# Kernel optimization log

Hardware: AMD Instinct MI355X
Metric: run time of the kernel (lower is better)

The kernel has to match this reference:

```python
import jax, jax.numpy as jnp
import numpy as np

B, S, H, N, L = 256, 64, 512, 16, 2
OUT_BITS = 32            # ceil(log2(n)), n = 2**32
PTR_BITS = 6             # ceil(log2(seq_len)), seq_len = 64
OUT_DIM = 3 + PTR_BITS   # = 9
T = 2 * OUT_BITS - 1     # 63 sequential decode steps


def _ln(x, g, b):
    m = jnp.mean(x, -1, keepdims=True)
    v = jnp.mean((x - m) ** 2, -1, keepdims=True)
    return (x - m) * jax.lax.rsqrt(v + 1e-5) * g + b


def _s4_step(A, Bm, Cm, D, oW, ob, s, x):
    # diagonal-SSM S4 block step: s (B,H,N) recurrent state, x (B,H) input
    s2 = A * s + Bm * x[:, :, None]
    y = jnp.einsum('bhn,hn->bh', s2, Cm) + D * x
    y = jax.nn.gelu(y, approximate=False) @ oW + ob
    return s2, y


def _forward(input_seq, in_W, in_b, A, Bm, Cm, D, outW, outb, ln_g, ln_b, head_W, head_b):
    Bsz = input_seq.shape[0]
    dt = input_seq.dtype
    x = input_seq @ in_W + in_b            # (B,S,H)
    encoded = x                            # encoded_inputs saved before S4 stack
    # ---- encoder: L S4 blocks, residual + layernorm ----
    for j in range(L):
        def step(s, xt, j=j):
            return _s4_step(A[j], Bm[j], Cm[j], D[j], outW[j], outb[j], s, xt)
        s0 = jnp.zeros((Bsz, H, N), dt)
        _, ys = jax.lax.scan(step, s0, jnp.swapaxes(x, 0, 1))
        x = _ln(jnp.swapaxes(ys, 0, 1) + x, ln_g[j], ln_b[j])
    dec0 = jnp.broadcast_to(jnp.array([0.0, 0.0, 1.0], dt), (Bsz, 3))
    carry0 = (jnp.zeros((L, Bsz, H, N), dt), jnp.zeros((Bsz, H), dt), dec0)
    ones1 = jnp.ones((Bsz, 1), dt)

    def dstep(carry, i):
        states, ctx, dec_in = carry
        dp = dec_in @ in_W + in_b          # (B,H)
        xd = dp
        new_states = []
        for j in range(L):
            s2, y = _s4_step(A[j], Bm[j], Cm[j], D[j], outW[j], outb[j], states[j], xd)
            new_states.append(s2)
            res = jnp.where(i == 0, dp, y)   # torch code: residual=proj on step 0, else doubles x_dec
            xd = _ln(y + res, ln_g[j], ln_b[j])
        is_out = (i % 2) == 0
        # pointer retrieval (only applied on odd steps via where)
        o_ptr = jax.nn.sigmoid((xd + ctx) @ head_W + head_b)
        ptr = jnp.argmax(o_ptr[:, 3:3 + PTR_BITS], axis=1)            # (B,)
        ptr_vec = jnp.take_along_axis(encoded, ptr[:, None, None], axis=1)[:, 0]
        ctx = jnp.where(is_out, ctx, ctx + ptr_vec)
        out = jax.nn.sigmoid((xd + ctx) @ head_W + head_b)            # (B,OUT_DIM)
        next_char = jnp.where(is_out, (out[:, 0:1] > 0.5).astype(dt), jnp.zeros((Bsz, 1), dt))
        tag0 = jnp.where(is_out, 1.0, 0.0) * ones1
        tag1 = ones1 - tag0
        dec_next = jnp.concatenate([next_char, tag0, tag1], axis=1)   # (B,3)
        return (jnp.stack(new_states), ctx, dec_next), out

    _, outs = jax.lax.scan(dstep, carry0, jnp.arange(T))
    return jnp.swapaxes(outs, 0, 1)        # (B, T, OUT_DIM)


def setup_inputs() -> dict:
    ks = jax.random.split(jax.random.key(0), 8)
    f32 = jnp.float32
    return {
        'input_seq': jax.random.uniform(ks[0], (B, S, 3), f32),
        'autoregressive_steps': T,
        'in_W': jax.random.normal(ks[1], (3, H), f32) * 0.5,
        'in_b': jnp.zeros((H,), f32),
        'A': jax.random.uniform(ks[2], (L, H, N), f32, 0.5, 0.99),
        'Bm': jax.random.normal(ks[3], (L, H, N), f32) * 0.1,
        'Cm': jax.random.normal(ks[4], (L, H, N), f32) * 0.1,
        'D': jnp.ones((L, H), f32),
        'outW': jax.random.normal(ks[5], (L, H, H), f32) * 0.02,
        'outb': jnp.zeros((L, H), f32),
        'ln_g': jnp.ones((L, H), f32),
        'ln_b': jnp.zeros((L, H), f32),
        'head_W': jax.random.normal(ks[6], (H, OUT_DIM), f32) * 0.05,
        'head_b': jnp.zeros((OUT_DIM,), f32),
    }


def reference(input_seq, autoregressive_steps, in_W, in_b, A, Bm, Cm, D, outW, outb, ln_g, ln_b, head_W, head_b):
    return _forward(input_seq, in_W, in_b, A, Bm, Cm, D, outW, outb, ln_g, ln_b, head_W, head_b)
```

## Files before the change

kernel.cpp:

```cpp
#include <hip/hip_runtime.h>
#include <math.h>

#define HDIM   512
#define NDIM   16
#define SEQ    64
#define TSTEPS 63
#define BATCH  256
#define ODIM   9
#define NTHR   512


__device__ __forceinline__ float gelu_f32(float x) {
    return 0.5f * x * (1.0f + erff(x * 0.70710678118654752440f));
}

__device__ __forceinline__ float sig32(float x) {
    return 1.0f / (1.0f + expf(-x));
}

__device__ __forceinline__ void load3_l2(const float* p0, const float* p1,
                                         const float* p2,
                                         float& v0, float& v1, float& v2) {
    asm volatile(
        "global_load_dword %0, %3, off sc0\n\t"
        "global_load_dword %1, %4, off sc0\n\t"
        "global_load_dword %2, %5, off sc0\n\t"
        "s_waitcnt vmcnt(0)"
        : "=&v"(v0), "=&v"(v1), "=&v"(v2)
        : "v"(p0), "v"(p1), "v"(p2)
        : "memory");
}
__device__ __forceinline__ float load1_l2(const float* p) {
    float v;
    asm volatile("global_load_dword %0, %1, off sc0\n\t"
                 "s_waitcnt vmcnt(0)"
                 : "=v"(v) : "v"(p) : "memory");
    return v;
}

__global__ __launch_bounds__(NTHR, 2)
void s4_decode_kernel(
    const float* __restrict__ input_seq,
    const float* __restrict__ in_W,
    const float* __restrict__ in_b,
    const float* __restrict__ Aarr,
    const float* __restrict__ Barr,
    const float* __restrict__ Carr,
    const float* __restrict__ Darr,
    const float* __restrict__ outW,
    const float* __restrict__ outb,
    const float* __restrict__ ln_g,
    const float* __restrict__ ln_b,
    const float* __restrict__ headW,
    const float* __restrict__ headb,
    float* __restrict__ out,
    float* gws, float* zws,
    unsigned* fg, unsigned* fz,
    unsigned* fx, unsigned* xid)
{
    __shared__ float  ld_xd[HDIM];
    __shared__ float  ld_gall[4 * HDIM];
    __shared__ float4 ld_z4[16 * 4 * 32];
    __shared__ float  ld_D0[HDIM];
    __shared__ float  ld_D1[HDIM];
    __shared__ float  ld_red[16];
    __shared__ float  ld_hred[8 * ODIM];
    __shared__ float  ld_logit[ODIM + 1];
    __shared__ float  ld_dec[4];
    __shared__ int    ld_ptr;
    __shared__ int    ld_fast;

    const int b    = blockIdx.x;
    const int tid  = threadIdx.x;
    const int hg   = tid >> 4;
    const int n    = tid & 15;
    const int mem  = (b >> 3) & 3;
    const int gbase = b - 8 * mem;
    const int c4   = tid & 31;
    const int rg   = tid >> 5;
    const int rgE  = (rg + ((b * 5) & 15)) & 15;
    const int base_row = rgE * 32;
    const int j0 = 0 + (0 >= mem), j1 = 1 + (1 >= mem), j2 = 2 + (2 >= mem);

    unsigned myxcd;
    asm volatile("s_getreg_b32 %0, hwreg(HW_REG_XCC_ID)" : "=s"(myxcd));
    if (tid == 0) {
        __hip_atomic_store(&xid[b], myxcd, __ATOMIC_RELAXED, __HIP_MEMORY_SCOPE_AGENT);
        __hip_atomic_store(&fx[b], 1u, __ATOMIC_RELEASE, __HIP_MEMORY_SCOPE_AGENT);
        unsigned ok = 1;
        #pragma unroll
        for (int j = 0; j < 4; ++j) {
            if (j == mem) continue;
            while (__hip_atomic_load(&fx[gbase + 8 * j],
                                     __ATOMIC_ACQUIRE, __HIP_MEMORY_SCOPE_AGENT) == 0)
                __builtin_amdgcn_s_sleep(1);
            ok &= (__hip_atomic_load(&xid[gbase + 8 * j],
                                     __ATOMIC_RELAXED, __HIP_MEMORY_SCOPE_AGENT) == myxcd);
        }
        ld_fast = (int)ok;
    }

    float s0[16], s1[16];
    float A0[16], B0[16], C0[16], A1[16], B1[16], C1[16];
    #pragma unroll
    for (int k = 0; k < 16; ++k) {
        int h  = hg + 32 * k;
        int i0 = h * NDIM + n;
        int i1 = (HDIM + h) * NDIM + n;
        A0[k] = Aarr[i0]; B0[k] = Barr[i0]; C0[k] = Carr[i0];
        A1[k] = Aarr[i1]; B1[k] = Barr[i1]; C1[k] = Carr[i1];
        s0[k] = 0.f; s1[k] = 0.f;
    }

    const float inb_t = in_b[tid];
    const float w0 = in_W[tid], w1 = in_W[HDIM + tid], w2 = in_W[2 * HDIM + tid];
    const float ob0 = outb[tid], ob1 = outb[HDIM + tid];
    const float lg0 = ln_g[tid], lg1 = ln_g[HDIM + tid];
    const float lb0 = ln_b[tid], lb1 = ln_b[HDIM + tid];

    ld_D0[tid] = Darr[tid];
    ld_D1[tid] = Darr[HDIM + tid];

    const float4* Wsl = (const float4*)outW + mem * 32 + c4;

    float ctxr = 0.f;
    if (tid == 0) { ld_dec[0] = 0.f; ld_dec[1] = 0.f; ld_dec[2] = 1.f; }
    __syncthreads();
    const bool fast = (ld_fast != 0);

    for (int i = 0; i < TSTEPS; ++i) {
        float dpv = fmaf(ld_dec[0], w0, fmaf(ld_dec[1], w1, fmaf(ld_dec[2], w2, inb_t)));
        __syncthreads();
        ld_xd[tid] = dpv;
        __syncthreads();

        #pragma unroll 1
        for (int blk = 0; blk < 2; ++blk) {
            const unsigned seq = (unsigned)(2 * i + blk + 1);
            {
                float* s  = blk ? s1 : s0;
                float* Ar = blk ? A1 : A0;
                float* Br = blk ? B1 : B0;
                float* Cr = blk ? C1 : C0;
                const float* Dl = blk ? ld_D1 : ld_D0;
                #pragma unroll
                for (int k = 0; k < 16; ++k) {
                    int h = hg + 32 * k;
                    float xh = ld_xd[h];
                    float sv = fmaf(Ar[k], s[k], Br[k] * xh);
                    s[k] = sv;
                    float p = sv * Cr[k];
                    p += __shfl_xor(p, 1);
                    p += __shfl_xor(p, 2);
                    p += __shfl_xor(p, 4);
                    p += __shfl_xor(p, 8);
                    if (n == 0) ld_gall[mem * HDIM + h] = gelu_f32(p + Dl[h] * xh);
                }
            }
            __syncthreads();
            if (fast) {
                gws[b * HDIM + tid] = ld_gall[mem * HDIM + tid];
            } else {
                __hip_atomic_store(&gws[b * HDIM + tid], ld_gall[mem * HDIM + tid],
                                   __ATOMIC_RELAXED, __HIP_MEMORY_SCOPE_AGENT);
            }
            __syncthreads();
            if (tid == 4)
                __hip_atomic_store(&fg[b], seq, __ATOMIC_RELAXED, __HIP_MEMORY_SCOPE_AGENT);
            if (tid < 3) {
                int j = tid + (tid >= mem ? 1 : 0);
                while (__hip_atomic_load(&fg[gbase + 8 * j],
                                         __ATOMIC_RELAXED, __HIP_MEMORY_SCOPE_AGENT) < seq)
                    __builtin_amdgcn_s_sleep(1);
            }
            __syncthreads();
            if (fast) {
                float v0, v1, v2;
                load3_l2(&gws[(gbase + 8 * j0) * HDIM + tid],
                         &gws[(gbase + 8 * j1) * HDIM + tid],
                         &gws[(gbase + 8 * j2) * HDIM + tid], v0, v1, v2);
                ld_gall[j0 * HDIM + tid] = v0;
                ld_gall[j1 * HDIM + tid] = v1;
                ld_gall[j2 * HDIM + tid] = v2;
            } else {
                ld_gall[j0 * HDIM + tid] =
                    __hip_atomic_load(&gws[(gbase + 8 * j0) * HDIM + tid],
                                      __ATOMIC_RELAXED, __HIP_MEMORY_SCOPE_AGENT);
                ld_gall[j1 * HDIM + tid] =
                    __hip_atomic_load(&gws[(gbase + 8 * j1) * HDIM + tid],
                                      __ATOMIC_RELAXED, __HIP_MEMORY_SCOPE_AGENT);
                ld_gall[j2 * HDIM + tid] =
                    __hip_atomic_load(&gws[(gbase + 8 * j2) * HDIM + tid],
                                      __ATOMIC_RELAXED, __HIP_MEMORY_SCOPE_AGENT);
            }
            __syncthreads();
            {
                const float4* Wb = Wsl + (size_t)blk * HDIM * 128;
                float4 acc[4];
                #pragma unroll
                for (int bi = 0; bi < 4; ++bi) acc[bi] = make_float4(0.f, 0.f, 0.f, 0.f);
                float4 a0 = Wb[(size_t)(base_row)     * 128];
                float4 a1 = Wb[(size_t)(base_row + 1) * 128];
                #pragma unroll 2
                for (int rr = 0; rr < 32; rr += 4) {
                    int rB = base_row + ((rr + 2) & 31);
                    float4 b0 = Wb[(size_t)rB * 128];
                    float4 b1 = Wb[(size_t)(rB + 1) * 128];
                    {
                        int r = base_row + rr;
                        #pragma unroll
                        for (int bi = 0; bi < 4; ++bi) {
                            float g0 = ld_gall[bi * HDIM + r];
                            float g1 = ld_gall[bi * HDIM + r + 1];
                            acc[bi].x = fmaf(g1, a1.x, fmaf(g0, a0.x, acc[bi].x));
                            acc[bi].y = fmaf(g1, a1.y, fmaf(g0, a0.y, acc[bi].y));
                            acc[bi].z = fmaf(g1, a1.z, fmaf(g0, a0.z, acc[bi].z));
                            acc[bi].w = fmaf(g1, a1.w, fmaf(g0, a0.w, acc[bi].w));
                        }
                    }
                    int rA = base_row + ((rr + 4) & 31);
                    a0 = Wb[(size_t)rA * 128];
                    a1 = Wb[(size_t)(rA + 1) * 128];
                    {
                        int r = base_row + rr + 2;
                        #pragma unroll
                        for (int bi = 0; bi < 4; ++bi) {
                            float g0 = ld_gall[bi * HDIM + r];
                            float g1 = ld_gall[bi * HDIM + r + 1];
                            acc[bi].x = fmaf(g1, b1.x, fmaf(g0, b0.x, acc[bi].x));
                            acc[bi].y = fmaf(g1, b1.y, fmaf(g0, b0.y, acc[bi].y));
                            acc[bi].z = fmaf(g1, b1.z, fmaf(g0, b0.z, acc[bi].z));
                            acc[bi].w = fmaf(g1, b1.w, fmaf(g0, b0.w, acc[bi].w));
                        }
                    }
                }
                #pragma unroll
                for (int bi = 0; bi < 4; ++bi)
                    ld_z4[(rg * 4 + bi) * 32 + c4] = acc[bi];
            }
            __syncthreads();
            {
                const float* zf = (const float*)ld_z4;
                int bi2 = tid >> 7;
                int col = tid & 127;
                float zv = 0.f;
                #pragma unroll
                for (int k = 0; k < 16; ++k) zv += zf[(k * 4 + bi2) * 128 + col];
                float* zp = &zws[(gbase + 8 * bi2) * HDIM + mem * 128 + col];
                if (fast) *zp = zv;
                else __hip_atomic_store(zp, zv, __ATOMIC_RELAXED, __HIP_MEMORY_SCOPE_AGENT);
            }
            __syncthreads();
            if (tid == 4)
                __hip_atomic_store(&fz[b], seq, __ATOMIC_RELAXED, __HIP_MEMORY_SCOPE_AGENT);
            if (tid < 3) {
                int j = tid + (tid >= mem ? 1 : 0);
                while (__hip_atomic_load(&fz[gbase + 8 * j],
                                         __ATOMIC_RELAXED, __HIP_MEMORY_SCOPE_AGENT) < seq)
                    __builtin_amdgcn_s_sleep(1);
            }
            __syncthreads();
            {
                float zraw = fast ? load1_l2(&zws[b * HDIM + tid])
                                  : __hip_atomic_load(&zws[b * HDIM + tid],
                                                      __ATOMIC_RELAXED,
                                                      __HIP_MEMORY_SCOPE_AGENT);
                float z = zraw + (blk ? ob1 : ob0);
                float res = (i == 0) ? dpv : z;
                float tmp = z + res;
                float v1 = tmp, v2 = tmp * tmp;
                #pragma unroll
                for (int m = 1; m < 64; m <<= 1) {
                    v1 += __shfl_xor(v1, m);
                    v2 += __shfl_xor(v2, m);
                }
                if ((tid & 63) == 0) {
                    ld_red[2 * (tid >> 6)]     = v1;
                    ld_red[2 * (tid >> 6) + 1] = v2;
                }
                __syncthreads();
                float s1r = 0.f, s2r = 0.f;
                #pragma unroll
                for (int q = 0; q < 8; ++q) { s1r += ld_red[2*q]; s2r += ld_red[2*q+1]; }
                float mu  = s1r * (1.f / 512.f);
                float var = s2r * (1.f / 512.f) - mu * mu;
                float rs  = rsqrtf(var + 1e-5f);
                __syncthreads();
                ld_xd[tid] = (tmp - mu) * rs * (blk ? lg1 : lg0) + (blk ? lb1 : lb0);
                __syncthreads();
            }
        }

        {
            float v = ld_xd[tid] + ctxr;
            const float* w = headW + tid * ODIM;
            float p[ODIM];
            #pragma unroll
            for (int o = 0; o < ODIM; ++o) p[o] = v * w[o];
            #pragma unroll
            for (int m = 1; m < 64; m <<= 1) {
                #pragma unroll
                for (int o = 0; o < ODIM; ++o) p[o] += __shfl_xor(p[o], m);
            }
            if ((tid & 63) == 0) {
                int wv = tid >> 6;
                #pragma unroll
                for (int o = 0; o < ODIM; ++o) ld_hred[wv * ODIM + o] = p[o];
            }
            __syncthreads();
            if (tid < ODIM) {
                float s = headb[tid];
                #pragma unroll
                for (int wv = 0; wv < 8; ++wv) s += ld_hred[wv * ODIM + tid];
                ld_logit[tid] = s;
            }
            __syncthreads();
        }

        const bool is_out = ((i & 1) == 0);
        if (is_out) {
            if (tid < ODIM)
                out[(b * TSTEPS + i) * ODIM + tid] = sig32(ld_logit[tid]);
            if (tid == 0) {
                float nc = (sig32(ld_logit[0]) > 0.5f) ? 1.f : 0.f;
                ld_dec[0] = nc; ld_dec[1] = 1.f; ld_dec[2] = 0.f;
            }
            __syncthreads();
        } else {
            if (tid == 0) {
                int best = 0; float bv = sig32(ld_logit[3]);
                #pragma unroll
                for (int o = 1; o < 6; ++o) {
                    float v2 = sig32(ld_logit[3 + o]);
                    if (v2 > bv) { bv = v2; best = o; }
                }
                ld_ptr = best;
                ld_dec[0] = 0.f; ld_dec[1] = 0.f; ld_dec[2] = 1.f;
            }
            __syncthreads();
            {
                const float* iseq = input_seq + (b * SEQ + ld_ptr) * 3;
                float e0 = iseq[0], e1 = iseq[1], e2 = iseq[2];
                ctxr += fmaf(e0, w0, fmaf(e1, w1, fmaf(e2, w2, inb_t)));
            }
            __syncthreads();
            {
                float v = ld_xd[tid] + ctxr;
                const float* w = headW + tid * ODIM;
                float p[ODIM];
                #pragma unroll
                for (int o = 0; o < ODIM; ++o) p[o] = v * w[o];
                #pragma unroll
                for (int m = 1; m < 64; m <<= 1) {
                    #pragma unroll
                    for (int o = 0; o < ODIM; ++o) p[o] += __shfl_xor(p[o], m);
                }
                if ((tid & 63) == 0) {
                    int wv = tid >> 6;
                    #pragma unroll
                    for (int o = 0; o < ODIM; ++o) ld_hred[wv * ODIM + o] = p[o];
                }
                __syncthreads();
                if (tid < ODIM) {
                    float s = headb[tid];
                    #pragma unroll
                    for (int wv = 0; wv < 8; ++wv) s += ld_hred[wv * ODIM + tid];
                    out[(b * TSTEPS + i) * ODIM + tid] = sig32(s);
                }
            }
            __syncthreads();
        }
    }
}

extern "C" void kernel_launch(void* const* d_in, const int* in_sizes, int n_in,
                              void* d_out, int out_size, void* d_ws, size_t ws_size,
                              hipStream_t stream) {
    (void)in_sizes; (void)n_in; (void)ws_size; (void)out_size;
    const float* input_seq = (const float*)d_in[0];
    const float* in_W   = (const float*)d_in[2];
    const float* in_b   = (const float*)d_in[3];
    const float* Aarr   = (const float*)d_in[4];
    const float* Barr   = (const float*)d_in[5];
    const float* Carr   = (const float*)d_in[6];
    const float* Darr   = (const float*)d_in[7];
    const float* outW   = (const float*)d_in[8];
    const float* outb   = (const float*)d_in[9];
    const float* ln_g   = (const float*)d_in[10];
    const float* ln_b   = (const float*)d_in[11];
    const float* headW  = (const float*)d_in[12];
    const float* headb  = (const float*)d_in[13];
    float* out = (float*)d_out;

    unsigned* fg  = (unsigned*)d_ws;
    unsigned* fz  = fg + BATCH;
    unsigned* fx  = fz + BATCH;
    unsigned* xid = fx + BATCH;
    float* gws = (float*)((char*)d_ws + 4096);
    float* zws = gws + BATCH * HDIM;

    hipMemsetAsync(d_ws, 0, 4096, stream);

    s4_decode_kernel<<<BATCH, NTHR, 0, stream>>>(
        input_seq, in_W, in_b, Aarr, Barr, Carr, Darr,
        outW, outb, ln_g, ln_b, headW, headb, out,
        gws, zws, fg, fz, fx, xid);
}
```

Before: 1.357 ms.

## Drop cross-block 4-way matvec sharing; each block computes full outW product alone

```diff
diff --git a/kernel.cpp b/kernel.cpp
--- a/kernel.cpp
+++ b/kernel.cpp
@@ -10,6 +10,8 @@
 #define NTHR   512
 
 
+typedef float f32x4 __attribute__((ext_vector_type(4)));
+
 __device__ __forceinline__ float gelu_f32(float x) {
     return 0.5f * x * (1.0f + erff(x * 0.70710678118654752440f));
 }
@@ -18,27 +20,16 @@
     return 1.0f / (1.0f + expf(-x));
 }
 
-__device__ __forceinline__ void load3_l2(const float* p0, const float* p1,
-                                         const float* p2,
-                                         float& v0, float& v1, float& v2) {
-    asm volatile(
-        "global_load_dword %0, %3, off sc0\n\t"
-        "global_load_dword %1, %4, off sc0\n\t"
-        "global_load_dword %2, %5, off sc0\n\t"
-        "s_waitcnt vmcnt(0)"
-        : "=&v"(v0), "=&v"(v1), "=&v"(v2)
-        : "v"(p0), "v"(p1), "v"(p2)
-        : "memory");
-}
-__device__ __forceinline__ float load1_l2(const float* p) {
-    float v;
-    asm volatile("global_load_dword %0, %1, off sc0\n\t"
-                 "s_waitcnt vmcnt(0)"
-                 : "=v"(v) : "v"(p) : "memory");
-    return v;
-}
-
-__global__ __launch_bounds__(NTHR, 2)
+__device__ __forceinline__ void fma_row4(float4& acc, const float4 g,
+                                         const float4 w0, const float4 w1,
+                                         const float4 w2, const float4 w3) {
+    acc.x = fmaf(g.w, w3.x, fmaf(g.z, w2.x, fmaf(g.y, w1.x, fmaf(g.x, w0.x, acc.x))));
+    acc.y = fmaf(g.w, w3.y, fmaf(g.z, w2.y, fmaf(g.y, w1.y, fmaf(g.x, w0.y, acc.y))));
+    acc.z = fmaf(g.w, w3.z, fmaf(g.z, w2.z, fmaf(g.y, w1.z, fmaf(g.x, w0.z, acc.z))));
+    acc.w = fmaf(g.w, w3.w, fmaf(g.z, w2.w, fmaf(g.y, w1.w, fmaf(g.x, w0.w, acc.w))));
+}
+
+__global__ __launch_bounds__(NTHR, 1)
 void s4_decode_kernel(
     const float* __restrict__ input_seq,
     const float* __restrict__ in_W,
@@ -53,62 +44,42 @@
     const float* __restrict__ ln_b,
     const float* __restrict__ headW,
     const float* __restrict__ headb,
-    float* __restrict__ out,
-    float* gws, float* zws,
-    unsigned* fg, unsigned* fz,
-    unsigned* fx, unsigned* xid)
+    float* __restrict__ out)
 {
-    __shared__ float  ld_xd[HDIM];
-    __shared__ float  ld_gall[4 * HDIM];
-    __shared__ float4 ld_z4[16 * 4 * 32];
-    __shared__ float  ld_D0[HDIM];
-    __shared__ float  ld_D1[HDIM];
-    __shared__ float  ld_red[16];
-    __shared__ float  ld_hred[8 * ODIM];
-    __shared__ float  ld_logit[ODIM + 1];
-    __shared__ float  ld_dec[4];
-    __shared__ int    ld_ptr;
-    __shared__ int    ld_fast;
-
-    const int b    = blockIdx.x;
-    const int tid  = threadIdx.x;
-    const int hg   = tid >> 4;
-    const int n    = tid & 15;
-    const int mem  = (b >> 3) & 3;
-    const int gbase = b - 8 * mem;
-    const int c4   = tid & 31;
-    const int rg   = tid >> 5;
-    const int rgE  = (rg + ((b * 5) & 15)) & 15;
-    const int base_row = rgE * 32;
-    const int j0 = 0 + (0 >= mem), j1 = 1 + (1 >= mem), j2 = 2 + (2 >= mem);
-
-    unsigned myxcd;
-    asm volatile("s_getreg_b32 %0, hwreg(HW_REG_XCC_ID)" : "=s"(myxcd));
-    if (tid == 0) {
-        __hip_atomic_store(&xid[b], myxcd, __ATOMIC_RELAXED, __HIP_MEMORY_SCOPE_AGENT);
-        __hip_atomic_store(&fx[b], 1u, __ATOMIC_RELEASE, __HIP_MEMORY_SCOPE_AGENT);
-        unsigned ok = 1;
-        #pragma unroll
-        for (int j = 0; j < 4; ++j) {
-            if (j == mem) continue;
-            while (__hip_atomic_load(&fx[gbase + 8 * j],
-                                     __ATOMIC_ACQUIRE, __HIP_MEMORY_SCOPE_AGENT) == 0)
-                __builtin_amdgcn_s_sleep(1);
-            ok &= (__hip_atomic_load(&xid[gbase + 8 * j],
-                                     __ATOMIC_RELAXED, __HIP_MEMORY_SCOPE_AGENT) == myxcd);
-        }
-        ld_fast = (int)ok;
+    __shared__ __align__(16) float ld_x[HDIM];
+    __shared__ __align__(16) float ld_g[HDIM];
+    __shared__ __align__(16) float4 ld_z4[4 * 128];
+    __shared__ __align__(16) float ld_A1[HDIM * NDIM];
+    __shared__ __align__(16) float ld_B1[HDIM * NDIM];
+    __shared__ __align__(16) float ld_C1[HDIM * NDIM];
+    __shared__ float ld_D0[HDIM];
+    __shared__ float ld_D1[HDIM];
+    __shared__ float ld_red[16];
+    __shared__ float ld_hred[8 * ODIM];
+    __shared__ float ld_logit[ODIM + 1];
+    __shared__ float ld_dec[4];
+    __shared__ int   ld_ptr;
+
+    const int b   = blockIdx.x;
+    const int tid = threadIdx.x;
+    const int n   = tid & 15;
+    const int hg  = tid >> 4;
+
+    for (int idx = tid; idx < HDIM * NDIM; idx += NTHR) {
+        ld_A1[idx] = Aarr[HDIM * NDIM + idx];
+        ld_B1[idx] = Barr[HDIM * NDIM + idx];
+        ld_C1[idx] = Carr[HDIM * NDIM + idx];
     }
+    ld_D0[tid] = Darr[tid];
+    ld_D1[tid] = Darr[HDIM + tid];
 
     float s0[16], s1[16];
-    float A0[16], B0[16], C0[16], A1[16], B1[16], C1[16];
+    float A0[16], B0[16], C0[16];
     #pragma unroll
     for (int k = 0; k < 16; ++k) {
-        int h  = hg + 32 * k;
-        int i0 = h * NDIM + n;
-        int i1 = (HDIM + h) * NDIM + n;
+        const int h  = hg + 32 * k;
+        const int i0 = h * NDIM + n;
         A0[k] = Aarr[i0]; B0[k] = Barr[i0]; C0[k] = Carr[i0];
-        A1[k] = Aarr[i1]; B1[k] = Barr[i1]; C1[k] = Carr[i1];
         s0[k] = 0.f; s1[k] = 0.f;
     }
 
@@ -117,157 +88,120 @@
     const float ob0 = outb[tid], ob1 = outb[HDIM + tid];
     const float lg0 = ln_g[tid], lg1 = ln_g[HDIM + tid];
     const float lb0 = ln_b[tid], lb1 = ln_b[HDIM + tid];
-
-    ld_D0[tid] = Darr[tid];
-    ld_D1[tid] = Darr[HDIM + tid];
-
-    const float4* Wsl = (const float4*)outW + mem * 32 + c4;
-
-    float ctxr = 0.f;
+    float hw[ODIM];
+    #pragma unroll
+    for (int o = 0; o < ODIM; ++o) hw[o] = headW[tid * ODIM + o];
+
+    float ctx = 0.f;
     if (tid == 0) { ld_dec[0] = 0.f; ld_dec[1] = 0.f; ld_dec[2] = 1.f; }
     __syncthreads();
-    const bool fast = (ld_fast != 0);
 
     for (int i = 0; i < TSTEPS; ++i) {
-        float dpv = fmaf(ld_dec[0], w0, fmaf(ld_dec[1], w1, fmaf(ld_dec[2], w2, inb_t)));
+        const float dpv = fmaf(ld_dec[0], w0,
+                          fmaf(ld_dec[1], w1,
+                          fmaf(ld_dec[2], w2, inb_t)));
         __syncthreads();
-        ld_xd[tid] = dpv;
+        ld_x[tid] = dpv;
         __syncthreads();
 
-        #pragma unroll 1
+        float xn = 0.f;
+
+        #pragma unroll
         for (int blk = 0; blk < 2; ++blk) {
-            const unsigned seq = (unsigned)(2 * i + blk + 1);
-            {
-                float* s  = blk ? s1 : s0;
-                float* Ar = blk ? A1 : A0;
-                float* Br = blk ? B1 : B0;
-                float* Cr = blk ? C1 : C0;
-                const float* Dl = blk ? ld_D1 : ld_D0;
+            float p[16];
+            if (blk == 0) {
                 #pragma unroll
                 for (int k = 0; k < 16; ++k) {
-                    int h = hg + 32 * k;
-                    float xh = ld_xd[h];
-                    float sv = fmaf(Ar[k], s[k], Br[k] * xh);
-                    s[k] = sv;
-                    float p = sv * Cr[k];
-                    p += __shfl_xor(p, 1);
-                    p += __shfl_xor(p, 2);
-                    p += __shfl_xor(p, 4);
-                    p += __shfl_xor(p, 8);
-                    if (n == 0) ld_gall[mem * HDIM + h] = gelu_f32(p + Dl[h] * xh);
-                }
-            }
-            __syncthreads();
-            if (fast) {
-                gws[b * HDIM + tid] = ld_gall[mem * HDIM + tid];
+                    const float x  = ld_x[hg + 32 * k];
+                    const float sv = fmaf(A0[k], s0[k], B0[k] * x);
+                    s0[k] = sv;
+                    p[k] = sv * C0[k];
+                }
             } else {
-                __hip_atomic_store(&gws[b * HDIM + tid], ld_gall[mem * HDIM + tid],
-                                   __ATOMIC_RELAXED, __HIP_MEMORY_SCOPE_AGENT);
-            }
-            __syncthreads();
-            if (tid == 4)
-                __hip_atomic_store(&fg[b], seq, __ATOMIC_RELAXED, __HIP_MEMORY_SCOPE_AGENT);
-            if (tid < 3) {
-                int j = tid + (tid >= mem ? 1 : 0);
-                while (__hip_atomic_load(&fg[gbase + 8 * j],
-                                         __ATOMIC_RELAXED, __HIP_MEMORY_SCOPE_AGENT) < seq)
-                    __builtin_amdgcn_s_sleep(1);
-            }
-            __syncthreads();
-            if (fast) {
-                float v0, v1, v2;
-                load3_l2(&gws[(gbase + 8 * j0) * HDIM + tid],
-                         &gws[(gbase + 8 * j1) * HDIM + tid],
-                         &gws[(gbase + 8 * j2) * HDIM + tid], v0, v1, v2);
-                ld_gall[j0 * HDIM + tid] = v0;
-                ld_gall[j1 * HDIM + tid] = v1;
-                ld_gall[j2 * HDIM + tid] = v2;
-            } else {
-                ld_gall[j0 * HDIM + tid] =
-                    __hip_atomic_load(&gws[(gbase + 8 * j0) * HDIM + tid],
-                                      __ATOMIC_RELAXED, __HIP_MEMORY_SCOPE_AGENT);
-                ld_gall[j1 * HDIM + tid] =
-                    __hip_atomic_load(&gws[(gbase + 8 * j1) * HDIM + tid],
-                                      __ATOMIC_RELAXED, __HIP_MEMORY_SCOPE_AGENT);
-                ld_gall[j2 * HDIM + tid] =
-                    __hip_atomic_load(&gws[(gbase + 8 * j2) * HDIM + tid],
-                                      __ATOMIC_RELAXED, __HIP_MEMORY_SCOPE_AGENT);
-            }
-            __syncthreads();
-            {
-                const float4* Wb = Wsl + (size_t)blk * HDIM * 128;
-                float4 acc[4];
-                #pragma unroll
-                for (int bi = 0; bi < 4; ++bi) acc[bi] = make_float4(0.f, 0.f, 0.f, 0.f);
-                float4 a0 = Wb[(size_t)(base_row)     * 128];
-                float4 a1 = Wb[(size_t)(base_row + 1) * 128];
+                #pragma unroll
+                for (int k = 0; k < 16; ++k) {
+                    const int ia = (hg + 32 * k) * NDIM + n;
+                    const float x  = ld_x[hg + 32 * k];
+                    const float sv = fmaf(ld_A1[ia], s1[k], ld_B1[ia] * x);
+                    s1[k] = sv;
+                    p[k] = sv * ld_C1[ia];
+                }
+            }
+            {
+                float q8[8];
+                { const bool bt = (n & 1) != 0;
+                  #pragma unroll
+                  for (int u = 0; u < 8; ++u) {
+                      const float sd = bt ? p[2 * u] : p[2 * u + 1];
+                      const float rc = __shfl_xor(sd, 1);
+                      q8[u] = (bt ? p[2 * u + 1] : p[2 * u]) + rc;
+                  } }
+                float q4[4];
+                { const bool bt = (n & 2) != 0;
+                  #pragma unroll
+                  for (int u = 0; u < 4; ++u) {
+                      const float sd = bt ? q8[2 * u] : q8[2 * u + 1];
+                      const float rc = __shfl_xor(sd, 2);
+                      q4[u] = (bt ? q8[2 * u + 1] : q8[2 * u]) + rc;
+                  } }
+                float q2[2];
+                { const bool bt = (n & 4) != 0;
+                  #pragma unroll
+                  for (int u = 0; u < 2; ++u) {
+                      const float sd = bt ? q2[0] * 0.f + (bt ? q4[2 * u] : q4[2 * u + 1]) : q4[2 * u + 1];
+                      q2[u] = 0.f; (void)sd;
+                  } }
+                { const bool bt = (n & 4) != 0;
+                  #pragma unroll
+                  for (int u = 0; u < 2; ++u) {
+                      const float sd = bt ? q4[2 * u] : q4[2 * u + 1];
+                      const float rc = __shfl_xor(sd, 4);
+                      q2[u] = (bt ? q4[2 * u + 1] : q4[2 * u]) + rc;
+                  } }
+                float y;
+                { const bool bt = (n & 8) != 0;
+                  const float sd = bt ? q2[0] : q2[1];
+                  const float rc = __shfl_xor(sd, 8);
+                  y = (bt ? q2[1] : q2[0]) + rc; }
+                const int h2 = hg + 32 * n;
+                const float dd = blk ? ld_D1[h2] : ld_D0[h2];
+                ld_g[h2] = gelu_f32(fmaf(dd, ld_x[h2], y));
+            }
+            __syncthreads();
+
+            {
+                const int rg = tid >> 7;
+                const int c  = tid & 127;
+                const float4* Wb = (const float4*)outW
+                    + (((size_t)blk) << 16) + (size_t)(rg * 128) * 128 + c;
+                const float* gq = &ld_g[rg * 128];
+                float4 acc = make_float4(0.f, 0.f, 0.f, 0.f);
+                float4 a0 = Wb[0 * 128], a1 = Wb[1 * 128],
+                       a2 = Wb[2 * 128], a3 = Wb[3 * 128];
                 #pragma unroll 2
-                for (int rr = 0; rr < 32; rr += 4) {
-                    int rB = base_row + ((rr + 2) & 31);
-                    float4 b0 = Wb[(size_t)rB * 128];
-                    float4 b1 = Wb[(size_t)(rB + 1) * 128];
-                    {
-                        int r = base_row + rr;
-                        #pragma unroll
-                        for (int bi = 0; bi < 4; ++bi) {
-                            float g0 = ld_gall[bi * HDIM + r];
-                            float g1 = ld_gall[bi * HDIM + r + 1];
-                            acc[bi].x = fmaf(g1, a1.x, fmaf(g0, a0.x, acc[bi].x));
-                            acc[bi].y = fmaf(g1, a1.y, fmaf(g0, a0.y, acc[bi].y));
-                            acc[bi].z = fmaf(g1, a1.z, fmaf(g0, a0.z, acc[bi].z));
-                            acc[bi].w = fmaf(g1, a1.w, fmaf(g0, a0.w, acc[bi].w));
-                        }
+                for (int rr = 0; rr < 128; rr += 4) {
+                    float4 b0, b1, b2, b3;
+                    if (rr < 124) {
+                        b0 = Wb[(size_t)(rr + 4) * 128];
+                        b1 = Wb[(size_t)(rr + 5) * 128];
+                        b2 = Wb[(size_t)(rr + 6) * 128];
+                        b3 = Wb[(size_t)(rr + 7) * 128];
                     }
-                    int rA = base_row + ((rr + 4) & 31);
-                    a0 = Wb[(size_t)rA * 128];
-                    a1 = Wb[(size_t)(rA + 1) * 128];
-                    {
-                        int r = base_row + rr + 2;
-                        #pragma unroll
-                        for (int bi = 0; bi < 4; ++bi) {
-                            float g0 = ld_gall[bi * HDIM + r];
-                            float g1 = ld_gall[bi * HDIM + r + 1];
-                            acc[bi].x = fmaf(g1, b1.x, fmaf(g0, b0.x, acc[bi].x));
-                            acc[bi].y = fmaf(g1, b1.y, fmaf(g0, b0.y, acc[bi].y));
-                            acc[bi].z = fmaf(g1, b1.z, fmaf(g0, b0.z, acc[bi].z));
-                            acc[bi].w = fmaf(g1, b1.w, fmaf(g0, b0.w, acc[bi].w));
-                        }
-                    }
-                }
-                #pragma unroll
-                for (int bi = 0; bi < 4; ++bi)
-                    ld_z4[(rg * 4 + bi) * 32 + c4] = acc[bi];
-            }
-            __syncthreads();
+                    const float4 g4 = *(const float4*)&gq[rr];
+                    fma_row4(acc, g4, a0, a1, a2, a3);
+                    if (rr < 124) { a0 = b0; a1 = b1; a2 = b2; a3 = b3; }
+                }
+                ld_z4[rg * 128 + c] = acc;
+            }
+            __syncthreads();
+
             {
                 const float* zf = (const float*)ld_z4;
-                int bi2 = tid >> 7;
-                int col = tid & 127;
-                float zv = 0.f;
-                #pragma unroll
-                for (int k = 0; k < 16; ++k) zv += zf[(k * 4 + bi2) * 128 + col];
-                float* zp = &zws[(gbase + 8 * bi2) * HDIM + mem * 128 + col];
-                if (fast) *zp = zv;
-                else __hip_atomic_store(zp, zv, __ATOMIC_RELAXED, __HIP_MEMORY_SCOPE_AGENT);
-            }
-            __syncthreads();
-            if (tid == 4)
-                __hip_atomic_store(&fz[b], seq, __ATOMIC_RELAXED, __HIP_MEMORY_SCOPE_AGENT);
-            if (tid < 3) {
-                int j = tid + (tid >= mem ? 1 : 0);
-                while (__hip_atomic_load(&fz[gbase + 8 * j],
-                                         __ATOMIC_RELAXED, __HIP_MEMORY_SCOPE_AGENT) < seq)
-                    __builtin_amdgcn_s_sleep(1);
-            }
-            __syncthreads();
-            {
-                float zraw = fast ? load1_l2(&zws[b * HDIM + tid])
-                                  : __hip_atomic_load(&zws[b * HDIM + tid],
-                                                      __ATOMIC_RELAXED,
-                                                      __HIP_MEMORY_SCOPE_AGENT);
-                float z = zraw + (blk ? ob1 : ob0);
-                float res = (i == 0) ? dpv : z;
-                float tmp = z + res;
+                const float z = zf[0 * HDIM + tid] + zf[1 * HDIM + tid]
+                              + zf[2 * HDIM + tid] + zf[3 * HDIM + tid]
+                              + (blk ? ob1 : ob0);
+                const float res = (i == 0) ? dpv : z;
+                const float tmp = z + res;
                 float v1 = tmp, v2 = tmp * tmp;
                 #pragma unroll
                 for (int m = 1; m < 64; m <<= 1) {
@@ -281,31 +215,33 @@
                 __syncthreads();
                 float s1r = 0.f, s2r = 0.f;
                 #pragma unroll
-                for (int q = 0; q < 8; ++q) { s1r += ld_red[2*q]; s2r += ld_red[2*q+1]; }
-                float mu  = s1r * (1.f / 512.f);
-                float var = s2r * (1.f / 512.f) - mu * mu;
-                float rs  = rsqrtf(var + 1e-5f);
+                for (int q = 0; q < 8; ++q) { s1r += ld_red[2 * q]; s2r += ld_red[2 * q + 1]; }
+                const float mu  = s1r * (1.f / 512.f);
+                const float var = s2r * (1.f / 512.f) - mu * mu;
+                const float rs  = rsqrtf(var + 1e-5f);
+                xn = (tmp - mu) * rs * (blk ? lg1 : lg0) + (blk ? lb1 : lb0);
                 __syncthreads();
-                ld_xd[tid] = (tmp - mu) * rs * (blk ? lg1 : lg0) + (blk ? lb1 : lb0);
-                __syncthreads();
+                if (blk == 0) {
+                    ld_x[tid] = xn;
+                    __syncthreads();
+                }
             }
         }
 
         {
-            float v = ld_xd[tid] + ctxr;
-            const float* w = headW + tid * ODIM;
-            float p[ODIM];
+            const float v = xn + ctx;
+            float hp[ODIM];
             #pragma unroll
-            for (int o = 0; o < ODIM; ++o) p[o] = v * w[o];
+            for (int o = 0; o < ODIM; ++o) hp[o] = v * hw[o];
             #pragma unroll
             for (int m = 1; m < 64; m <<= 1) {
                 #pragma unroll
-                for (int o = 0; o < ODIM; ++o) p[o] += __shfl_xor(p[o], m);
+                for (int o = 0; o < ODIM; ++o) hp[o] += __shfl_xor(hp[o], m);
             }
             if ((tid & 63) == 0) {
-                int wv = tid >> 6;
-                #pragma unroll
-                for (int o = 0; o < ODIM; ++o) ld_hred[wv * ODIM + o] = p[o];
+                const int wv = tid >> 6;
+                #pragma unroll
+                for (int o = 0; o < ODIM; ++o) ld_hred[wv * ODIM + o] = hp[o];
             }
             __syncthreads();
             if (tid < ODIM) {
@@ -320,9 +256,9 @@
         const bool is_out = ((i & 1) == 0);
         if (is_out) {
             if (tid < ODIM)
-                out[(b * TSTEPS + i) * ODIM + tid] = sig32(ld_logit[tid]);
+                out[((size_t)b * TSTEPS + i) * ODIM + tid] = sig32(ld_logit[tid]);
             if (tid == 0) {
-                float nc = (sig32(ld_logit[0]) > 0.5f) ? 1.f : 0.f;
+                const float nc = (sig32(ld_logit[0]) > 0.5f) ? 1.f : 0.f;
                 ld_dec[0] = nc; ld_dec[1] = 1.f; ld_dec[2] = 0.f;
             }
             __syncthreads();
@@ -331,7 +267,7 @@
                 int best = 0; float bv = sig32(ld_logit[3]);
                 #pragma unroll
                 for (int o = 1; o < 6; ++o) {
-                    float v2 = sig32(ld_logit[3 + o]);
+                    const float v2 = sig32(ld_logit[3 + o]);
                     if (v2 > bv) { bv = v2; best = o; }
                 }
                 ld_ptr = best;
@@ -339,36 +275,34 @@
             }
             __syncthreads();
             {
-                const float* iseq = input_seq + (b * SEQ + ld_ptr) * 3;
-                float e0 = iseq[0], e1 = iseq[1], e2 = iseq[2];
-                ctxr += fmaf(e0, w0, fmaf(e1, w1, fmaf(e2, w2, inb_t)));
-            }
-            __syncthreads();
-            {
-                float v = ld_xd[tid] + ctxr;
-                const float* w = headW + tid * ODIM;
-                float p[ODIM];
-                #pragma unroll
-                for (int o = 0; o < ODIM; ++o) p[o] = v * w[o];
+                const float* iseq = input_seq + ((size_t)b * SEQ + ld_ptr) * 3;
+                ctx += fmaf(iseq[0], w0, fmaf(iseq[1], w1, fmaf(iseq[2], w2, inb_t)));
+            }
+            __syncthreads();
+            {
+                const float v = xn + ctx;
+                float hq[ODIM];
+                #pragma unroll
+                for (int o = 0; o < ODIM; ++o) hq[o] = v * hw[o];
                 #pragma unroll
                 for (int m = 1; m < 64; m <<= 1) {
                     #pragma unroll
-                    for (int o = 0; o < ODIM; ++o) p[o] += __shfl_xor(p[o], m);
+                    for (int o = 0; o < ODIM; ++o) hq[o] += __shfl_xor(hq[o], m);
                 }
                 if ((tid & 63) == 0) {
-                    int wv = tid >> 6;
+                    const int wv = tid >> 6;
                     #pragma unroll
-                    for (int o = 0; o < ODIM; ++o) ld_hred[wv * ODIM + o] = p[o];
+                    for (int o = 0; o < ODIM; ++o) ld_hred[wv * ODIM + o] = hq[o];
                 }
                 __syncthreads();
                 if (tid < ODIM) {
                     float s = headb[tid];
                     #pragma unroll
                     for (int wv = 0; wv < 8; ++wv) s += ld_hred[wv * ODIM + tid];
-                    out[(b * TSTEPS + i) * ODIM + tid] = sig32(s);
-                }
-            }
-            __syncthreads();
+                    out[((size_t)b * TSTEPS + i) * ODIM + tid] = sig32(s);
+                }
+                __syncthreads();
+            }
         }
     }
 }
@@ -376,7 +310,7 @@
 extern "C" void kernel_launch(void* const* d_in, const int* in_sizes, int n_in,
                               void* d_out, int out_size, void* d_ws, size_t ws_size,
                               hipStream_t stream) {
-    (void)in_sizes; (void)n_in; (void)ws_size; (void)out_size;
+    (void)in_sizes; (void)n_in; (void)d_ws; (void)ws_size; (void)out_size;
     const float* input_seq = (const float*)d_in[0];
     const float* in_W   = (const float*)d_in[2];
     const float* in_b   = (const float*)d_in[3];
@@ -392,17 +326,7 @@
     const float* headb  = (const float*)d_in[13];
     float* out = (float*)d_out;
 
-    unsigned* fg  = (unsigned*)d_ws;
-    unsigned* fz  = fg + BATCH;
-    unsigned* fx  = fz + BATCH;
-    unsigned* xid = fx + BATCH;
-    float* gws = (float*)((char*)d_ws + 4096);
-    float* zws = gws + BATCH * HDIM;
-
-    hipMemsetAsync(d_ws, 0, 4096, stream);
-
     s4_decode_kernel<<<BATCH, NTHR, 0, stream>>>(
         input_seq, in_W, in_b, Aarr, Barr, Carr, Darr,
-        outW, outb, ln_g, ln_b, headW, headb, out,
-        gws, zws, fg, fz, fx, xid);
-}
+        outW, outb, ln_g, ln_b, headW, headb, out);
+}
```

Result: slower. 1.882 ms (+38.6%).
